# Optimization experiments

Hardware: AMD Instinct MI355X
Metric: run time of the kernel (lower is better)

Reference implementation:

```python
import jax, jax.numpy as jnp
import numpy as np

EPS = 1e-12  # matches torch F.normalize eps

def _l2norm(v, axis):
    n = jnp.sqrt(jnp.sum(v * v, axis=axis, keepdims=True))
    return v / jnp.maximum(n, EPS)

def setup_inputs() -> dict:
    key = jax.random.key(0)
    kx, kc = jax.random.split(key)
    B, C, H, W, N = 16, 512, 96, 96, 27
    x = jax.random.normal(kx, (B, C, H, W), dtype=jnp.float32)
    clusters = jax.random.normal(kc, (N, C), dtype=jnp.float32)
    alpha = jnp.full((1,), 8.0, dtype=jnp.float32)  # softmax temperature
    return {"x": x, "clusters": clusters, "alpha": alpha}

def reference(x, clusters, alpha):
    # L2-normalize features along channel dim and clusters along feature dim
    normed_clusters = _l2norm(clusters, axis=1)          # [N, C]
    normed_features = _l2norm(x, axis=1)                 # [B, C, H, W]
    # cosine similarity: [B, N, H, W]
    inner_products = jnp.einsum('bchw,nc->bnhw', normed_features, normed_clusters)
    a = alpha.reshape(())
    cluster_probs = jax.nn.softmax(inner_products * a, axis=1)
    cluster_loss = -jnp.mean(jnp.sum(cluster_probs * inner_products, axis=1))
    return (cluster_loss, cluster_probs)
```

## Files before the change

### kernel.cpp

```cpp
#include <hip/hip_runtime.h>
#include <math.h>

#define NCL  27
#define CCH  512
#define HWPX 9216
#define NB   16
#define NPIX (NB * HWPX)
#define EPSN 1e-12f
#define NCHK 32

typedef short        short8 __attribute__((ext_vector_type(8)));
typedef unsigned int uint4v __attribute__((ext_vector_type(4)));
typedef float        f32x16 __attribute__((ext_vector_type(16)));

__device__ __forceinline__ unsigned short f2bf(float f) {
    unsigned u = __float_as_uint(f);
    return (unsigned short)((u + 0x7fffu + ((u >> 16) & 1u)) >> 16);
}
__device__ __forceinline__ float bf2f(unsigned short h) {
    return __uint_as_float(((unsigned)h) << 16);
}

__global__ __launch_bounds__(64) void k0_prep(const float* __restrict__ cl,
                                              unsigned short* __restrict__ clAhi,
                                              unsigned short* __restrict__ clAlo,
                                              float* __restrict__ loss_acc) {
    const int n = blockIdx.x;
    const int t = threadIdx.x;
    float inv = 0.f;
    if (n < NCL) {
        const float* row = cl + n * CCH;
        float ss = 0.f;
#pragma unroll
        for (int i = 0; i < CCH / 64; ++i) {
            float v = row[i * 64 + t];
            ss = fmaf(v, v, ss);
        }
#pragma unroll
        for (int off = 32; off > 0; off >>= 1)
            ss += __shfl_xor(ss, off, 64);
        inv = 1.0f / fmaxf(sqrtf(ss), EPSN);
    }
    const int chunk = t >> 1;
    const int half  = t & 1;
    const int lane  = n + 32 * half;
    const size_t base = ((size_t)chunk * 64 + lane) * 8;
#pragma unroll
    for (int j = 0; j < 8; ++j) {
        const int k = chunk * 16 + 8 * half + j;
        float v = (n < NCL) ? cl[n * CCH + k] * inv : 0.f;
        unsigned short h = f2bf(v);
        float lo = v - bf2f(h);
        clAhi[base + j] = h;
        clAlo[base + j] = f2bf(lo);
    }
    if (n == 0 && t < 32) loss_acc[t * 32] = 0.f;
}

__global__ __launch_bounds__(64) void k1_main(const float* __restrict__ x,
                                              const unsigned short* __restrict__ clAhi,
                                              const unsigned short* __restrict__ clAlo,
                                              const float* __restrict__ alpha_p,
                                              float* __restrict__ out,
                                              float* __restrict__ loss_acc) {
    const int l    = threadIdx.x;
    const int px0  = blockIdx.x * 32;
    const int b    = px0 / HWPX;
    const int hw0  = px0 - b * HWPX;
    const int col  = l & 31;
    const int half = l >> 5;

    const float* xg = x + ((size_t)b * CCH + 8 * half) * HWPX + hw0 + col;
    const unsigned short* pAh = clAhi + (size_t)l * 8;
    const unsigned short* pAl = clAlo + (size_t)l * 8;

    f32x16 acc = {0.f, 0.f, 0.f, 0.f, 0.f, 0.f, 0.f, 0.f,
                  0.f, 0.f, 0.f, 0.f, 0.f, 0.f, 0.f, 0.f};
    float ss = 0.f;

#pragma unroll 2
    for (int t = 0; t < NCHK; ++t) {
        float xv[8];
#pragma unroll
        for (int j = 0; j < 8; ++j)
            xv[j] = xg[(size_t)(t * 16 + j) * HWPX];

        short8 ah = *(const short8*)(pAh + (size_t)t * 512);
        short8 al = *(const short8*)(pAl + (size_t)t * 512);

        unsigned hb[8], ub[8], lb[8];
#pragma unroll
        for (int j = 0; j < 8; ++j) {
            ss = fmaf(xv[j], xv[j], ss);
            ub[j] = __float_as_uint(xv[j]);
            hb[j] = ub[j] & 0xFFFF0000u;
            lb[j] = __float_as_uint(xv[j] - __uint_as_float(hb[j]));
        }
        uint4v bhp, blp;
#pragma unroll
        for (int i = 0; i < 4; ++i) {
            bhp[i] = (ub[2 * i] >> 16) | hb[2 * i + 1];
            blp[i] = (lb[2 * i] >> 16) | (lb[2 * i + 1] & 0xFFFF0000u);
        }
        short8 bh = __builtin_bit_cast(short8, bhp);
        short8 bl = __builtin_bit_cast(short8, blp);

        acc = __builtin_amdgcn_mfma_f32_32x32x16_bf16(ah, bh, acc, 0, 0, 0);
        acc = __builtin_amdgcn_mfma_f32_32x32x16_bf16(al, bh, acc, 0, 0, 0);
        acc = __builtin_amdgcn_mfma_f32_32x32x16_bf16(ah, bl, acc, 0, 0, 0);
    }

    ss += __shfl_xor(ss, 32, 64);
    const float inv_x = 1.0f / fmaxf(sqrtf(ss), EPSN);
    const float alpha = alpha_p[0];

    float ip[16], ex[16];
#pragma unroll
    for (int r = 0; r < 16; ++r) {
        ip[r] = acc[r] * inv_x;
        ex[r] = ip[r] * alpha;
    }

    float m = -1e30f;
#pragma unroll
    for (int r = 0; r < 12; ++r) m = fmaxf(m, ex[r]);
    if (half == 0) {
#pragma unroll
        for (int r = 12; r < 15; ++r) m = fmaxf(m, ex[r]);
    }
    m = fmaxf(m, __shfl_xor(m, 32, 64));

    float sum = 0.f;
#pragma unroll
    for (int r = 0; r < 12; ++r) {
        ex[r] = __expf(ex[r] - m);
        sum += ex[r];
    }
#pragma unroll
    for (int r = 12; r < 16; ++r) {
        float e = (half == 0 && r < 15) ? __expf(ex[r] - m) : 0.f;
        ex[r] = e;
        sum += e;
    }
    sum += __shfl_xor(sum, 32, 64);
    const float inv_sum = 1.0f / sum;

    float lterm = 0.f;
    float* ob = out + 1 + (size_t)b * (NCL * HWPX) + hw0 + col;
#pragma unroll
    for (int r = 0; r < 16; ++r) {
        const int row = (r & 3) + 8 * (r >> 2) + 4 * half;
        if (r < 12 || (half == 0 && r < 15)) {
            float pr = ex[r] * inv_sum;
            ob[(size_t)row * HWPX] = pr;
            lterm = fmaf(pr, ip[r], lterm);
        }
    }

#pragma unroll
    for (int off = 32; off > 0; off >>= 1)
        lterm += __shfl_xor(lterm, off, 64);
    if (l == 0)
        atomicAdd(&loss_acc[(blockIdx.x & 31) * 32], lterm);
}

__global__ void k2_fin(const float* __restrict__ loss_acc,
                       float* __restrict__ out) {
    float s = 0.f;
#pragma unroll
    for (int i = 0; i < 32; ++i) s += loss_acc[i * 32];
    out[0] = -s * (1.0f / (float)NPIX);
}

extern "C" void kernel_launch(void* const* d_in, const int* in_sizes, int n_in,
                              void* d_out, int out_size, void* d_ws, size_t ws_size,
                              hipStream_t stream) {
    const float* x     = (const float*)d_in[0];
    const float* cl    = (const float*)d_in[1];
    const float* alpha = (const float*)d_in[2];
    float* out = (float*)d_out;

    float*          loss_acc = (float*)d_ws;
    unsigned short* clAhi    = (unsigned short*)((char*)d_ws + 4096);
    unsigned short* clAlo    = clAhi + 32 * 64 * 8;

    hipLaunchKernelGGL(k0_prep, dim3(32), dim3(64), 0, stream,
                       cl, clAhi, clAlo, loss_acc);
    hipLaunchKernelGGL(k1_main, dim3(NPIX / 32), dim3(64), 0, stream,
                       x, clAhi, clAlo, alpha, out, loss_acc);
    hipLaunchKernelGGL(k2_fin, dim3(1), dim3(1), 0, stream, loss_acc, out);
}
```

Baseline: 82.92 us.

## Stage x tiles through LDS with async global_load_lds double buffering

The main kernel now uses 256-thread blocks covering 128 pixels, four wavefronts each handling 32 pixels. Each channel chunk of x is copied straight into a double-buffered LDS tile with the async global-to-LDS load builtin, and the next chunk is prefetched while MFMAs run on the current one. The goal is wider 16-byte coalesced loads and overlap of memory latency with compute. The cost is a block-wide barrier on every iteration and extra LDS traffic.

```diff
diff --git a/kernel.cpp b/kernel.cpp
--- a/kernel.cpp
+++ b/kernel.cpp
@@ -8,9 +8,9 @@
 #define NPIX (NB * HWPX)
 #define EPSN 1e-12f
 #define NCHK 32
+#define PXT  128
 
 typedef short        short8 __attribute__((ext_vector_type(8)));
-typedef unsigned int uint4v __attribute__((ext_vector_type(4)));
 typedef float        f32x16 __attribute__((ext_vector_type(16)));
 
 __device__ __forceinline__ unsigned short f2bf(float f) {
@@ -19,6 +19,13 @@
 }
 __device__ __forceinline__ float bf2f(unsigned short h) {
     return __uint_as_float(((unsigned)h) << 16);
+}
+
+__device__ __forceinline__ void gload_lds16(const float* g, float* lds) {
+    __builtin_amdgcn_global_load_lds(
+        (const __attribute__((address_space(1))) unsigned int*)g,
+        (__attribute__((address_space(3))) unsigned int*)lds,
+        16, 0, 0);
 }
 
 __global__ __launch_bounds__(64) void k0_prep(const float* __restrict__ cl,
@@ -57,36 +64,53 @@
     if (n == 0 && t < 32) loss_acc[t * 32] = 0.f;
 }
 
-__global__ __launch_bounds__(64) void k1_main(const float* __restrict__ x,
-                                              const unsigned short* __restrict__ clAhi,
-                                              const unsigned short* __restrict__ clAlo,
-                                              const float* __restrict__ alpha_p,
-                                              float* __restrict__ out,
-                                              float* __restrict__ loss_acc) {
-    const int l    = threadIdx.x;
-    const int px0  = blockIdx.x * 32;
+__global__ __launch_bounds__(256) void k1_main(const float* __restrict__ x,
+                                               const unsigned short* __restrict__ clAhi,
+                                               const unsigned short* __restrict__ clAlo,
+                                               const float* __restrict__ alpha_p,
+                                               float* __restrict__ out,
+                                               float* __restrict__ loss_acc) {
+    __shared__ float xt[2][16][PXT];
+
+    const int tid  = threadIdx.x;
+    const int l    = tid & 63;
+    const int w    = tid >> 6;
+    const int px0  = blockIdx.x * PXT;
     const int b    = px0 / HWPX;
     const int hw0  = px0 - b * HWPX;
     const int col  = l & 31;
     const int half = l >> 5;
 
-    const float* xg = x + ((size_t)b * CCH + 8 * half) * HWPX + hw0 + col;
+    const float* xsrc = x + ((size_t)b * CCH + 4 * w + (l >> 5)) * HWPX
+                          + hw0 + (l & 31) * 4;
     const unsigned short* pAh = clAhi + (size_t)l * 8;
     const unsigned short* pAl = clAlo + (size_t)l * 8;
+
+#define STAGE(tc, bf)                                                         \
+    {                                                                         \
+        gload_lds16(xsrc + ((size_t)(tc) * 16 + 0) * HWPX, &xt[bf][4 * w][0]);\
+        gload_lds16(xsrc + ((size_t)(tc) * 16 + 2) * HWPX, &xt[bf][4 * w + 2][0]);\
+    }
 
     f32x16 acc = {0.f, 0.f, 0.f, 0.f, 0.f, 0.f, 0.f, 0.f,
                   0.f, 0.f, 0.f, 0.f, 0.f, 0.f, 0.f, 0.f};
     float ss = 0.f;
 
+    STAGE(0, 0);
+    __syncthreads();
+
+    int buf = 0;
 #pragma unroll 2
     for (int t = 0; t < NCHK; ++t) {
-        float xv[8];
-#pragma unroll
-        for (int j = 0; j < 8; ++j)
-            xv[j] = xg[(size_t)(t * 16 + j) * HWPX];
-
         short8 ah = *(const short8*)(pAh + (size_t)t * 512);
         short8 al = *(const short8*)(pAl + (size_t)t * 512);
+
+        if (t + 1 < NCHK) STAGE(t + 1, buf ^ 1);
+
+        float xv[8];
+#pragma unroll
+        for (int j = 0; j < 8; ++j)
+            xv[j] = xt[buf][8 * half + j][32 * w + col];
 
         unsigned hb[8], ub[8], lb[8];
 #pragma unroll
@@ -96,19 +120,29 @@
             hb[j] = ub[j] & 0xFFFF0000u;
             lb[j] = __float_as_uint(xv[j] - __uint_as_float(hb[j]));
         }
-        uint4v bhp, blp;
+        unsigned bhp[4], blp[4];
 #pragma unroll
         for (int i = 0; i < 4; ++i) {
             bhp[i] = (ub[2 * i] >> 16) | hb[2 * i + 1];
             blp[i] = (lb[2 * i] >> 16) | (lb[2 * i + 1] & 0xFFFF0000u);
         }
-        short8 bh = __builtin_bit_cast(short8, bhp);
-        short8 bl = __builtin_bit_cast(short8, blp);
+        short8 bh, bl;
+#pragma unroll
+        for (int i = 0; i < 4; ++i) {
+            bh[2 * i]     = (short)(bhp[i] & 0xFFFFu);
+            bh[2 * i + 1] = (short)(bhp[i] >> 16);
+            bl[2 * i]     = (short)(blp[i] & 0xFFFFu);
+            bl[2 * i + 1] = (short)(blp[i] >> 16);
+        }
 
         acc = __builtin_amdgcn_mfma_f32_32x32x16_bf16(ah, bh, acc, 0, 0, 0);
         acc = __builtin_amdgcn_mfma_f32_32x32x16_bf16(al, bh, acc, 0, 0, 0);
         acc = __builtin_amdgcn_mfma_f32_32x32x16_bf16(ah, bl, acc, 0, 0, 0);
-    }
+
+        __syncthreads();
+        buf ^= 1;
+    }
+#undef STAGE
 
     ss += __shfl_xor(ss, 32, 64);
     const float inv_x = 1.0f / fmaxf(sqrtf(ss), EPSN);
@@ -146,7 +180,7 @@
     const float inv_sum = 1.0f / sum;
 
     float lterm = 0.f;
-    float* ob = out + 1 + (size_t)b * (NCL * HWPX) + hw0 + col;
+    float* ob = out + 1 + (size_t)b * (NCL * HWPX) + hw0 + 32 * w + col;
 #pragma unroll
     for (int r = 0; r < 16; ++r) {
         const int row = (r & 3) + 8 * (r >> 2) + 4 * half;
@@ -161,7 +195,7 @@
     for (int off = 32; off > 0; off >>= 1)
         lterm += __shfl_xor(lterm, off, 64);
     if (l == 0)
-        atomicAdd(&loss_acc[(blockIdx.x & 31) * 32], lterm);
+        atomicAdd(&loss_acc[((blockIdx.x & 7) * 4 + w) * 32], lterm);
 }
 
 __global__ void k2_fin(const float* __restrict__ loss_acc,
@@ -186,7 +220,7 @@
 
     hipLaunchKernelGGL(k0_prep, dim3(32), dim3(64), 0, stream,
                        cl, clAhi, clAlo, loss_acc);
-    hipLaunchKernelGGL(k1_main, dim3(NPIX / 32), dim3(64), 0, stream,
+    hipLaunchKernelGGL(k1_main, dim3(NPIX / PXT), dim3(256), 0, stream,
                        x, clAhi, clAlo, alpha, out, loss_acc);
     hipLaunchKernelGGL(k2_fin, dim3(1), dim3(1), 0, stream, loss_acc, out);
 }
```

Result: faster. 68.42 us, median of 2 (-17.5%).

## Stage x tiles into LDS via direct global-to-LDS loads with double buffering

Applied to the files above, without the earlier changes.

The x chunk loads in the main GEMM loop move from per-lane strided global loads into registers to `global_load_lds` DMA transfers of 16 bytes per lane into two LDS tiles. The loop becomes a double-buffered software pipeline: the next chunk is staged while the current one is read back from LDS, split into bf16 hi/lo parts and fed to the MFMAs, using manual `s_waitcnt vmcnt` fences. The aim is wider, more coalesced loads and overlap of memory latency with compute. The cost is an extra LDS round trip. The scheme also holds fewer bytes in flight per wave than the old unrolled register loads and relies on hand-written wait counts being correct.

```diff
diff --git a/kernel.cpp b/kernel.cpp
--- a/kernel.cpp
+++ b/kernel.cpp
@@ -10,7 +10,6 @@
 #define NCHK 32
 
 typedef short        short8 __attribute__((ext_vector_type(8)));
-typedef unsigned int uint4v __attribute__((ext_vector_type(4)));
 typedef float        f32x16 __attribute__((ext_vector_type(16)));
 
 __device__ __forceinline__ unsigned short f2bf(float f) {
@@ -19,6 +18,13 @@
 }
 __device__ __forceinline__ float bf2f(unsigned short h) {
     return __uint_as_float(((unsigned)h) << 16);
+}
+
+__device__ __forceinline__ void gload_lds16(const float* g, float* lds) {
+    __builtin_amdgcn_global_load_lds(
+        (const __attribute__((address_space(1))) unsigned int*)g,
+        (__attribute__((address_space(3))) unsigned int*)lds,
+        16, 0, 0);
 }
 
 __global__ __launch_bounds__(64) void k0_prep(const float* __restrict__ cl,
@@ -57,12 +63,51 @@
     if (n == 0 && t < 32) loss_acc[t * 32] = 0.f;
 }
 
+__device__ __forceinline__ void compute_chunk(const float (*buf)[32],
+                                              short8 ah, short8 al,
+                                              f32x16& acc, float& ss,
+                                              int col, int half) {
+    float xv[8];
+#pragma unroll
+    for (int j = 0; j < 8; ++j)
+        xv[j] = buf[8 * half + j][col];
+
+    unsigned hb[8], ub[8], lb[8];
+#pragma unroll
+    for (int j = 0; j < 8; ++j) {
+        ss = fmaf(xv[j], xv[j], ss);
+        ub[j] = __float_as_uint(xv[j]);
+        hb[j] = ub[j] & 0xFFFF0000u;
+        lb[j] = __float_as_uint(xv[j] - __uint_as_float(hb[j]));
+    }
+    unsigned bhp[4], blp[4];
+#pragma unroll
+    for (int i = 0; i < 4; ++i) {
+        bhp[i] = (ub[2 * i] >> 16) | hb[2 * i + 1];
+        blp[i] = (lb[2 * i] >> 16) | (lb[2 * i + 1] & 0xFFFF0000u);
+    }
+    short8 bh, bl;
+#pragma unroll
+    for (int i = 0; i < 4; ++i) {
+        bh[2 * i]     = (short)(bhp[i] & 0xFFFFu);
+        bh[2 * i + 1] = (short)(bhp[i] >> 16);
+        bl[2 * i]     = (short)(blp[i] & 0xFFFFu);
+        bl[2 * i + 1] = (short)(blp[i] >> 16);
+    }
+    acc = __builtin_amdgcn_mfma_f32_32x32x16_bf16(ah, bh, acc, 0, 0, 0);
+    acc = __builtin_amdgcn_mfma_f32_32x32x16_bf16(al, bh, acc, 0, 0, 0);
+    acc = __builtin_amdgcn_mfma_f32_32x32x16_bf16(ah, bl, acc, 0, 0, 0);
+}
+
 __global__ __launch_bounds__(64) void k1_main(const float* __restrict__ x,
                                               const unsigned short* __restrict__ clAhi,
                                               const unsigned short* __restrict__ clAlo,
                                               const float* __restrict__ alpha_p,
                                               float* __restrict__ out,
                                               float* __restrict__ loss_acc) {
+    __shared__ float xtA[16][32];
+    __shared__ float xtB[16][32];
+
     const int l    = threadIdx.x;
     const int px0  = blockIdx.x * 32;
     const int b    = px0 / HWPX;
@@ -70,45 +115,49 @@
     const int col  = l & 31;
     const int half = l >> 5;
 
-    const float* xg = x + ((size_t)b * CCH + 8 * half) * HWPX + hw0 + col;
+    const float* xsrc = x + ((size_t)b * CCH + (l >> 3)) * HWPX
+                          + hw0 + (l & 7) * 4;
     const unsigned short* pAh = clAhi + (size_t)l * 8;
     const unsigned short* pAl = clAlo + (size_t)l * 8;
+
+#define STAGE(tc, dst)                                                    \
+    {                                                                     \
+        gload_lds16(xsrc + (size_t)(tc) * 16 * HWPX,       &dst[0][0]);   \
+        gload_lds16(xsrc + ((size_t)(tc) * 16 + 8) * HWPX, &dst[8][0]);   \
+    }
 
     f32x16 acc = {0.f, 0.f, 0.f, 0.f, 0.f, 0.f, 0.f, 0.f,
                   0.f, 0.f, 0.f, 0.f, 0.f, 0.f, 0.f, 0.f};
     float ss = 0.f;
 
-#pragma unroll 2
-    for (int t = 0; t < NCHK; ++t) {
-        float xv[8];
-#pragma unroll
-        for (int j = 0; j < 8; ++j)
-            xv[j] = xg[(size_t)(t * 16 + j) * HWPX];
-
-        short8 ah = *(const short8*)(pAh + (size_t)t * 512);
-        short8 al = *(const short8*)(pAl + (size_t)t * 512);
-
-        unsigned hb[8], ub[8], lb[8];
-#pragma unroll
-        for (int j = 0; j < 8; ++j) {
-            ss = fmaf(xv[j], xv[j], ss);
-            ub[j] = __float_as_uint(xv[j]);
-            hb[j] = ub[j] & 0xFFFF0000u;
-            lb[j] = __float_as_uint(xv[j] - __uint_as_float(hb[j]));
-        }
-        uint4v bhp, blp;
-#pragma unroll
-        for (int i = 0; i < 4; ++i) {
-            bhp[i] = (ub[2 * i] >> 16) | hb[2 * i + 1];
-            blp[i] = (lb[2 * i] >> 16) | (lb[2 * i + 1] & 0xFFFF0000u);
-        }
-        short8 bh = __builtin_bit_cast(short8, bhp);
-        short8 bl = __builtin_bit_cast(short8, blp);
-
-        acc = __builtin_amdgcn_mfma_f32_32x32x16_bf16(ah, bh, acc, 0, 0, 0);
-        acc = __builtin_amdgcn_mfma_f32_32x32x16_bf16(al, bh, acc, 0, 0, 0);
-        acc = __builtin_amdgcn_mfma_f32_32x32x16_bf16(ah, bl, acc, 0, 0, 0);
-    }
+    STAGE(0, xtA);
+
+    for (int t = 0; t < NCHK - 2; t += 2) {
+        short8 ah0 = *(const short8*)(pAh + (size_t)t * 512);
+        short8 al0 = *(const short8*)(pAl + (size_t)t * 512);
+        STAGE(t + 1, xtB);
+        asm volatile("s_waitcnt vmcnt(4)" ::: "memory");
+        compute_chunk(xtA, ah0, al0, acc, ss, col, half);
+
+        short8 ah1 = *(const short8*)(pAh + (size_t)(t + 1) * 512);
+        short8 al1 = *(const short8*)(pAl + (size_t)(t + 1) * 512);
+        STAGE(t + 2, xtA);
+        asm volatile("s_waitcnt vmcnt(4)" ::: "memory");
+        compute_chunk(xtB, ah1, al1, acc, ss, col, half);
+    }
+    {
+        short8 ah0 = *(const short8*)(pAh + (size_t)30 * 512);
+        short8 al0 = *(const short8*)(pAl + (size_t)30 * 512);
+        STAGE(31, xtB);
+        asm volatile("s_waitcnt vmcnt(4)" ::: "memory");
+        compute_chunk(xtA, ah0, al0, acc, ss, col, half);
+
+        short8 ah1 = *(const short8*)(pAh + (size_t)31 * 512);
+        short8 al1 = *(const short8*)(pAl + (size_t)31 * 512);
+        asm volatile("s_waitcnt vmcnt(0)" ::: "memory");
+        compute_chunk(xtB, ah1, al1, acc, ss, col, half);
+    }
+#undef STAGE
 
     ss += __shfl_xor(ss, 32, 64);
     const float inv_x = 1.0f / fmaxf(sqrtf(ss), EPSN);
```

Measured after the change: 85.00 us. 1.03x slower.
